# Kernel tuning notes

Hardware: AMD Instinct MI355X
Metric: run time of the kernel (lower is better)

## Reference

```python
import jax, jax.numpy as jnp
import numpy as np

B, S_LONG, S_SHORT, C_IN, H, D_STATE = 16384, 100, 10, 4, 64, 16
BN_EPS = 1e-5


def setup_inputs() -> dict:
    key = jax.random.key(0)
    ks = jax.random.split(key, 32)
    n = lambda i, shape, s=0.1: (jax.random.normal(ks[i], shape, dtype=jnp.float32) * s)
    inp = {
        "x": jax.random.normal(ks[0], (B, S_LONG, C_IN), dtype=jnp.float32),
        # ConvolutionalEyes (Conv1d weights are [out, in, k])
        "conv1_w": n(1, (H, C_IN, 3)), "conv1_b": n(2, (H,)),
        "conv2_w": n(3, (H, H, 5)),    "conv2_b": n(4, (H,)),
        "conv3_w": n(5, (H, H, 7)),    "conv3_b": n(6, (H,)),
        # BatchNorm1d (eval mode: running_mean=0, running_var=1)
        "bn1_g": jnp.ones((H,)), "bn1_b": jnp.zeros((H,)),
        "bn2_g": jnp.ones((H,)), "bn2_b": jnp.zeros((H,)),
        "bn3_g": jnp.ones((H,)), "bn3_b": jnp.zeros((H,)),
        # input_proj
        "proj_w": n(7, (C_IN, H)), "proj_b": n(8, (H,)),
        # MambaBlock (proj_in exists in torch code but is unused in forward)
        "A": n(9, (D_STATE, D_STATE)),
        "Bm": n(10, (H, D_STATE)),
        "Cm": n(11, (D_STATE, H)),
        "out_w": n(12, (H, H)), "out_b": n(13, (H,)),
        # ContextualGate
        "g1_w": n(14, (2 * H, H)), "g1_b": n(15, (H,)),
        "g2_w": n(16, (H, H)),     "g2_b": n(17, (H,)),
        # trading head
        "h1_w": n(18, (H, 32)), "h1_b": n(19, (32,)),
        "h2_w": n(20, (32, 3)), "h2_b": n(21, (3,)),
    }
    return inp


def _conv_bn_relu(x, w, b, g, beta, pad):
    # x: [B, C, L], w: [O, I, K]
    y = jax.lax.conv_general_dilated(x, w, (1,), [(pad, pad)],
                                     dimension_numbers=("NCW", "OIW", "NCW"))
    y = y + b[None, :, None]
    # eval-mode BN with running_mean=0, running_var=1
    y = g[None, :, None] * y * jax.lax.rsqrt(jnp.float32(1.0 + BN_EPS)) + beta[None, :, None]
    return jax.nn.relu(y)


def reference(x, conv1_w, conv1_b, conv2_w, conv2_b, conv3_w, conv3_b,
              bn1_g, bn1_b, bn2_g, bn2_b, bn3_g, bn3_b,
              proj_w, proj_b, A, Bm, Cm, out_w, out_b,
              g1_w, g1_b, g2_w, g2_b, h1_w, h1_b, h2_w, h2_b):
    # --- split windows ---
    x_short = x[:, -S_SHORT:, :]          # [B, 10, 4]
    x_long = x                            # [B, 100, 4]

    # --- ConvolutionalEyes (dropout = identity in eval) ---
    xc = jnp.swapaxes(x_short, 1, 2)      # [B, 4, 10]
    xc = _conv_bn_relu(xc, conv1_w, conv1_b, bn1_g, bn1_b, 1)
    xc = _conv_bn_relu(xc, conv2_w, conv2_b, bn2_g, bn2_b, 2)
    xc = _conv_bn_relu(xc, conv3_w, conv3_b, bn3_g, bn3_b, 3)
    short_features = jnp.mean(xc, axis=2)  # [B, 64]

    # --- input projection ---
    xp = x_long @ proj_w + proj_b          # [B, 100, 64]

    # --- MambaBlock: sequential scan over time ---
    def step(h, x_t):                      # h: [B, 16], x_t: [B, 64]
        h = jnp.tanh(x_t @ Bm + h @ A.T)
        return h, h @ Cm                   # y_t: [B, 64]

    h0 = jnp.zeros((x.shape[0], D_STATE), dtype=x.dtype)
    _, ys = jax.lax.scan(step, h0, jnp.swapaxes(xp, 0, 1))  # ys: [100, B, 64]
    long_context = ys[-1] @ out_w + out_b  # proj_out applied, last timestep

    # --- ContextualGate ---
    combined = jnp.concatenate([short_features, long_context], axis=1)  # [B, 128]
    gate = jax.nn.sigmoid(jnp.tanh(combined @ g1_w + g1_b) @ g2_w + g2_b)
    filtered = short_features * gate

    # --- trading head (dropout = identity in eval) ---
    logits = jax.nn.relu(filtered @ h1_w + h1_b) @ h2_w + h2_b  # [B, 3]
    return logits
```

## Files before the change

### kernel.cpp

```cpp
#include <hip/hip_runtime.h>
#include <cstddef>

#define NB 16384
#define NRNN (NB/64)

typedef __attribute__((ext_vector_type(8))) _Float16 half8;
typedef __attribute__((ext_vector_type(4))) _Float16 half4;
typedef __attribute__((ext_vector_type(4))) float f32x4;
typedef __attribute__((ext_vector_type(2))) float f32x2;
typedef __attribute__((ext_vector_type(16))) float f32x16;

#define OFF_W1T 0
#define OFF_SC1 768
#define OFF_SH1 832
#define OFF_SC2 896
#define OFF_SH2 960
#define OFF_SC3 1024
#define OFF_SH3 1088
#define OFF_PB  1152
#define OFF_PBB 1216
#define OFF_W2H 2304
#define OFF_W2L 12544
#define OFF_W3H 22784
#define OFF_W3L 37120
#define OFF_SF  51456
#define OFF_H   (51456 + NB*64)
#define OFF_TF  1362176

#define G1H 0
#define G1L 8192
#define G2H 16384
#define G2L 20480
#define H1H 24576
#define H1L 26624
#define H2H 28672
#define H2L 29184
#define COH 29696
#define COL 30720
#define TFH 31744

static __device__ __forceinline__ f32x16 mfma32(half8 a, half8 b, f32x16 c) {
  return __builtin_amdgcn_mfma_f32_32x32x16_f16(a, b, c, 0, 0, 0);
}
static __device__ __forceinline__ f32x4 mfma16(half4 a, half4 b, f32x4 c) {
  return __builtin_amdgcn_mfma_f32_16x16x16f16(a, b, c, 0, 0, 0);
}
static __device__ __forceinline__ f32x4 mfma16k32(half8 a, half8 b, f32x4 c) {
  return __builtin_amdgcn_mfma_f32_16x16x32_f16(a, b, c, 0, 0, 0);
}

__global__ __launch_bounds__(256) void prep_kernel(
    const float* __restrict__ conv1_w, const float* __restrict__ conv1_b,
    const float* __restrict__ conv2_w, const float* __restrict__ conv2_b,
    const float* __restrict__ conv3_w, const float* __restrict__ conv3_b,
    const float* __restrict__ bn1_g, const float* __restrict__ bn1_b,
    const float* __restrict__ bn2_g, const float* __restrict__ bn2_b,
    const float* __restrict__ bn3_g, const float* __restrict__ bn3_b,
    const float* __restrict__ proj_w, const float* __restrict__ proj_b,
    const float* __restrict__ A, const float* __restrict__ Bm,
    const float* __restrict__ Cm, const float* __restrict__ out_w,
    const float* __restrict__ g1_w, const float* __restrict__ g2_w,
    const float* __restrict__ h1_w, const float* __restrict__ h2_w,
    float* __restrict__ ws)
{
  int tid = blockIdx.x * blockDim.x + threadIdx.x;
  int nt = gridDim.x * blockDim.x;
  const float s = rsqrtf(1.0f + 1e-5f);

  for (int i = tid; i < 64*12; i += nt) {
    int o = i & 63, rk = i >> 6;
    ws[OFF_W1T + i] = conv1_w[o*12 + rk];
  }
  for (int o = tid; o < 64; o += nt) {
    float s1 = bn1_g[o]*s, s2 = bn2_g[o]*s, s3 = bn3_g[o]*s;
    ws[OFF_SC1+o] = s1; ws[OFF_SH1+o] = s1*conv1_b[o] + bn1_b[o];
    ws[OFF_SC2+o] = s2; ws[OFF_SH2+o] = s2*conv2_b[o] + bn2_b[o];
    ws[OFF_SC3+o] = s3; ws[OFF_SH3+o] = s3*conv3_b[o] + bn3_b[o];
  }
  {
    _Float16* w2h = (_Float16*)(ws + OFF_W2H);
    _Float16* w2l = (_Float16*)(ws + OFF_W2L);
    for (int i = tid; i < 20*2*64; i += nt) {
      int lane = i & 63, ot = (i >> 6) & 1, sk = i >> 7;
      int tap = sk >> 2, ic0 = (sk & 3)*16 + (lane >> 5)*8;
      int o = ot*32 + (lane & 31);
      #pragma unroll
      for (int j = 0; j < 8; ++j) {
        float w = conv2_w[o*320 + (ic0 + j)*5 + tap];
        _Float16 hi = (_Float16)w;
        w2h[(size_t)i*8 + j] = hi;
        w2l[(size_t)i*8 + j] = (_Float16)(w - (float)hi);
      }
    }
  }
  {
    _Float16* w3h = (_Float16*)(ws + OFF_W3H);
    _Float16* w3l = (_Float16*)(ws + OFF_W3L);
    for (int i = tid; i < 28*2*64; i += nt) {
      int lane = i & 63, ot = (i >> 6) & 1, sk = i >> 7;
      int tap = sk >> 2, ic0 = (sk & 3)*16 + (lane >> 5)*8;
      int o = ot*32 + (lane & 31);
      #pragma unroll
      for (int j = 0; j < 8; ++j) {
        float w = conv3_w[o*448 + (ic0 + j)*7 + tap];
        _Float16 hi = (_Float16)w;
        w3h[(size_t)i*8 + j] = hi;
        w3l[(size_t)i*8 + j] = (_Float16)(w - (float)hi);
      }
    }
  }
  for (int i = tid; i < 64; i += nt) {
    int c = i >> 4, j = i & 15;
    float acc = 0.f;
    for (int m = 0; m < 64; ++m) acc += proj_w[c*64+m]*Bm[m*16+j];
    ws[OFF_PB + i] = acc;
  }
  for (int j = tid; j < 16; j += nt) {
    float acc = 0.f;
    for (int m = 0; m < 64; ++m) acc += proj_b[m]*Bm[m*16+j];
    ws[OFF_PBB + j] = acc;
  }

  _Float16* tf = (_Float16*)(ws + OFF_TF);
  for (int i = tid; i < 16*64; i += nt) {
    int l = i & 63, f = i >> 6, mt = f >> 2, ks = f & 3;
    int o = mt*16 + (l & 15), kb = ks*32 + (l >> 4)*8;
    #pragma unroll
    for (int j = 0; j < 8; ++j) {
      float w = g1_w[(size_t)(kb + j)*64 + o];
      _Float16 hi = (_Float16)w;
      tf[G1H + (size_t)i*8 + j] = hi;
      tf[G1L + (size_t)i*8 + j] = (_Float16)(w - (float)hi);
    }
  }
  for (int i = tid; i < 8*64; i += nt) {
    int l = i & 63, f = i >> 6, mt = f >> 1, ks = f & 1;
    int o = mt*16 + (l & 15), kb = ks*32 + (l >> 4)*8;
    #pragma unroll
    for (int j = 0; j < 8; ++j) {
      float w = g2_w[(size_t)(kb + j)*64 + o];
      _Float16 hi = (_Float16)w;
      tf[G2H + (size_t)i*8 + j] = hi;
      tf[G2L + (size_t)i*8 + j] = (_Float16)(w - (float)hi);
    }
  }
  for (int i = tid; i < 4*64; i += nt) {
    int l = i & 63, f = i >> 6, mt = f >> 1, ks = f & 1;
    int hx = mt*16 + (l & 15), kb = ks*32 + (l >> 4)*8;
    #pragma unroll
    for (int j = 0; j < 8; ++j) {
      float w = h1_w[(size_t)(kb + j)*32 + hx];
      _Float16 hi = (_Float16)w;
      tf[H1H + (size_t)i*8 + j] = hi;
      tf[H1L + (size_t)i*8 + j] = (_Float16)(w - (float)hi);
    }
  }
  for (int i = tid; i < 64; i += nt) {
    int l = i, m = l & 15, kb = (l >> 4)*8;
    #pragma unroll
    for (int j = 0; j < 8; ++j) {
      float w = (m < 3) ? h2_w[(size_t)(kb + j)*3 + m] : 0.f;
      _Float16 hi = (_Float16)w;
      tf[H2H + (size_t)i*8 + j] = hi;
      tf[H2L + (size_t)i*8 + j] = (_Float16)(w - (float)hi);
    }
  }
  for (int i = tid; i < 4*64; i += nt) {
    int l = i & 63, mt = i >> 6;
    int o = mt*16 + (l & 15), kb = (l >> 4)*4;
    #pragma unroll
    for (int j = 0; j < 4; ++j) {
      float acc = 0.f;
      for (int m = 0; m < 64; ++m) acc += Cm[(kb + j)*64 + m]*out_w[m*64 + o];
      _Float16 hi = (_Float16)acc;
      tf[COH + (size_t)i*4 + j] = hi;
      tf[COL + (size_t)i*4 + j] = (_Float16)(acc - (float)hi);
    }
  }
}

__global__ __launch_bounds__(256, 4) void conv123_kernel(
    const float* __restrict__ x, const float* __restrict__ wsr,
    const float* __restrict__ A, float* __restrict__ hout,
    float* __restrict__ sfp)
{
  __shared__ __align__(16) _Float16 ah[16][640], al[16][640];

  const int tid = threadIdx.x;
  const int lane = tid & 63;
  const int wid = tid >> 6;

  if (blockIdx.x < NRNN) {
    const int colb = lane & 15;
    const int q = lane >> 4;
    const size_t b = ((size_t)blockIdx.x*4 + wid)*16 + colb;

    const f32x4 av = *(const f32x4*)(A + (size_t)(lane & 15)*16 + q*4);
    half4 Ahi, Alo;
    #pragma unroll
    for (int j = 0; j < 4; ++j) {
      _Float16 hi = (_Float16)av[j];
      Ahi[j] = hi;
      Alo[j] = (_Float16)(av[j] - (float)hi);
    }
    f32x4 pb0 = *(const f32x4*)(wsr + OFF_PB + 0*16 + q*4);
    f32x4 pb1 = *(const f32x4*)(wsr + OFF_PB + 1*16 + q*4);
    f32x4 pb2 = *(const f32x4*)(wsr + OFF_PB + 2*16 + q*4);
    f32x4 pb3 = *(const f32x4*)(wsr + OFF_PB + 3*16 + q*4);
    f32x4 pbb = *(const f32x4*)(wsr + OFF_PBB + q*4);

    const float* xb = x + b*400;
    half4 hh = {}, hl = {};
    f32x4 hf;
    #pragma unroll 4
    for (int t = 0; t < 100; ++t) {
      const f32x4 xv = *(const f32x4*)(xb + t*4);
      f32x4 U;
      #pragma unroll
      for (int r = 0; r < 4; ++r)
        U[r] = pbb[r] + xv[0]*pb0[r] + xv[1]*pb1[r] + xv[2]*pb2[r] + xv[3]*pb3[r];
      f32x4 u = mfma16(Alo, hh, U);
      u = mfma16(Ahi, hl, u);
      u = mfma16(Ahi, hh, u);
      #pragma unroll
      for (int r = 0; r < 4; ++r) {
        float e = __expf(2.f*u[r]);
        float hn = 1.f - 2.f/(e + 1.f);
        hf[r] = hn;
        _Float16 hi = (_Float16)hn;
        hh[r] = hi;
        hl[r] = (_Float16)(hn - (float)hi);
      }
    }
    *(f32x4*)(hout + b*16 + q*4) = hf;
    return;
  }

  const int n = lane & 15;
  const int nc = (n < 10) ? n : 9;
  const int cbK = (lane >> 5);
  const int rq = 4 * (lane >> 5);
  const int lbA = 4*wid + ((lane >> 4) & 1);
  const int lbB = lbA + 2;
  const half8 z8 = {};
  const size_t B0g = (size_t)(blockIdx.x - NRNN) * 16;

  {
    const float sc1 = wsr[OFF_SC1 + lane], sh1 = wsr[OFF_SH1 + lane];
    const int lc = lane >> 3, lo7 = lane & 7;
    #pragma unroll
    for (int bb = 0; bb < 4; ++bb) {
      const int lb = 4*wid + bb;
      const size_t gb = B0g + lb;
      float xv[4][12];
      #pragma unroll
      for (int c = 0; c < 4; ++c) { xv[c][0] = 0.f; xv[c][11] = 0.f; }
      #pragma unroll
      for (int tt = 0; tt < 10; ++tt) {
        const f32x4 xt = *(const f32x4*)(x + gb*400 + (90 + tt)*4);
        #pragma unroll
        for (int c = 0; c < 4; ++c) xv[c][1 + tt] = xt[c];
      }
      float a1[10];
      #pragma unroll
      for (int t = 0; t < 10; ++t) a1[t] = 0.f;
      #pragma unroll
      for (int c = 0; c < 4; ++c)
        #pragma unroll
        for (int k = 0; k < 3; ++k) {
          const float wv = wsr[OFF_W1T + (c*3 + k)*64 + lane];
          #pragma unroll
          for (int t = 0; t < 10; ++t) a1[t] += wv * xv[c][t + k];
        }
      #pragma unroll
      for (int t = 0; t < 10; ++t) {
        float v = sc1*a1[t] + sh1;
        v = v > 0.f ? v : 0.f;
        _Float16 hi = (_Float16)v;
        const int sw = t*64 + (((lc ^ (t & 7)) << 3) | lo7);
        ah[lb][sw] = hi;
        al[lb][sw] = (_Float16)(v - (float)hi);
      }
    }
  }

  const _Float16* bhpA = &ah[lbA][0];
  const _Float16* blpA = &al[lbA][0];
  const _Float16* bhpB = &ah[lbB][0];
  const _Float16* blpB = &al[lbB][0];
  const _Float16* w2h = (const _Float16*)(wsr + OFF_W2H);
  const _Float16* w2l = (const _Float16*)(wsr + OFF_W2L);
  const _Float16* w3h = (const _Float16*)(wsr + OFF_W3H);
  const _Float16* w3l = (const _Float16*)(wsr + OFF_W3L);
  const int lw8 = lane*8;

  f32x16 a0A, a1A, a0B, a1B;
  {
    #pragma unroll
    for (int r = 0; r < 16; ++r) { a0A[r] = 0.f; a1A[r] = 0.f; a0B[r] = 0.f; a1B[r] = 0.f; }
    #pragma unroll
    for (int sk = 0; sk < 20; ++sk) {
      const int tap = sk >> 2;
      const int cb = (sk & 3)*2 + cbK;
      const int t = nc + tap - 2;
      const int tc = t < 0 ? 0 : (t > 9 ? 9 : t);
      const bool valid = (t >= 0) & (t <= 9);
      const int off = tc*64 + ((cb ^ (tc & 7)) << 3);
      half8 bhA = *(const half8*)(bhpA + off);
      half8 blA = *(const half8*)(blpA + off);
      half8 bhB = *(const half8*)(bhpB + off);
      half8 blB = *(const half8*)(blpB + off);
      bhA = valid ? bhA : z8;
      blA = valid ? blA : z8;
      bhB = valid ? bhB : z8;
      blB = valid ? blB : z8;
      const half8 wh0 = *(const half8*)(w2h + (size_t)(sk*2 + 0)*512 + lw8);
      const half8 wh1 = *(const half8*)(w2h + (size_t)(sk*2 + 1)*512 + lw8);
      const half8 wl0 = *(const half8*)(w2l + (size_t)(sk*2 + 0)*512 + lw8);
      const half8 wl1 = *(const half8*)(w2l + (size_t)(sk*2 + 1)*512 + lw8);
      a0A = mfma32(wh0, bhA, a0A);
      a0A = mfma32(wh0, blA, a0A);
      a0A = mfma32(wl0, bhA, a0A);
      a1A = mfma32(wh1, bhA, a1A);
      a1A = mfma32(wh1, blA, a1A);
      a1A = mfma32(wl1, bhA, a1A);
      a0B = mfma32(wh0, bhB, a0B);
      a0B = mfma32(wh0, blB, a0B);
      a0B = mfma32(wl0, bhB, a0B);
      a1B = mfma32(wh1, bhB, a1B);
      a1B = mfma32(wh1, blB, a1B);
      a1B = mfma32(wl1, bhB, a1B);
    }
    if (n < 10) {
      const int n7 = n & 7;
      auto epi = [&](const f32x16& ac, int ot, int lb) {
        #pragma unroll
        for (int q = 0; q < 4; ++q) {
          const int rowb = 8*q + rq + ot*32;
          const f32x4 sc = *(const f32x4*)(wsr + OFF_SC2 + rowb);
          const f32x4 sh = *(const f32x4*)(wsr + OFF_SH2 + rowb);
          half4 h4, l4;
          #pragma unroll
          for (int r = 0; r < 4; ++r) {
            float v = sc[r]*ac[4*q + r] + sh[r];
            v = v > 0.f ? v : 0.f;
            _Float16 hi = (_Float16)v;
            h4[r] = hi;
            l4[r] = (_Float16)(v - (float)hi);
          }
          const int sw = n*64 + (((((q + 4*ot) ^ n7)) << 3) | rq);
          *(half4*)(&ah[lb][sw]) = h4;
          *(half4*)(&al[lb][sw]) = l4;
        }
      };
      epi(a0A, 0, lbA);
      epi(a1A, 1, lbA);
      epi(a0B, 0, lbB);
      epi(a1B, 1, lbB);
    }
  }

  {
    f32x16 b0A, b1A, b0B, b1B;
    #pragma unroll
    for (int r = 0; r < 16; ++r) { b0A[r] = 0.f; b1A[r] = 0.f; b0B[r] = 0.f; b1B[r] = 0.f; }
    #pragma unroll
    for (int sk = 0; sk < 28; ++sk) {
      const int tap = sk >> 2;
      const int cb = (sk & 3)*2 + cbK;
      const int t = nc + tap - 3;
      const int tc = t < 0 ? 0 : (t > 9 ? 9 : t);
      const bool valid = (t >= 0) & (t <= 9);
      const int off = tc*64 + ((cb ^ (tc & 7)) << 3);
      half8 bhA = *(const half8*)(bhpA + off);
      half8 blA = *(const half8*)(blpA + off);
      half8 bhB = *(const half8*)(bhpB + off);
      half8 blB = *(const half8*)(blpB + off);
      bhA = valid ? bhA : z8;
      blA = valid ? blA : z8;
      bhB = valid ? bhB : z8;
      blB = valid ? blB : z8;
      const half8 wh0 = *(const half8*)(w3h + (size_t)(sk*2 + 0)*512 + lw8);
      const half8 wh1 = *(const half8*)(w3h + (size_t)(sk*2 + 1)*512 + lw8);
      const half8 wl0 = *(const half8*)(w3l + (size_t)(sk*2 + 0)*512 + lw8);
      const half8 wl1 = *(const half8*)(w3l + (size_t)(sk*2 + 1)*512 + lw8);
      b0A = mfma32(wh0, bhA, b0A);
      b0A = mfma32(wh0, blA, b0A);
      b0A = mfma32(wl0, bhA, b0A);
      b1A = mfma32(wh1, bhA, b1A);
      b1A = mfma32(wh1, blA, b1A);
      b1A = mfma32(wl1, bhA, b1A);
      b0B = mfma32(wh0, bhB, b0B);
      b0B = mfma32(wh0, blB, b0B);
      b0B = mfma32(wl0, bhB, b0B);
      b1B = mfma32(wh1, bhB, b1B);
      b1B = mfma32(wh1, blB, b1B);
      b1B = mfma32(wl1, bhB, b1B);
    }
    auto epi = [&](const f32x16& ac, int ot, int lb) {
      #pragma unroll
      for (int q = 0; q < 4; ++q) {
        const int rowb = 8*q + rq + ot*32;
        const f32x4 sc = *(const f32x4*)(wsr + OFF_SC3 + rowb);
        const f32x4 sh = *(const f32x4*)(wsr + OFF_SH3 + rowb);
        f32x4 v;
        #pragma unroll
        for (int r = 0; r < 4; ++r) {
          float t2 = sc[r]*ac[4*q + r] + sh[r];
          t2 = t2 > 0.f ? t2 : 0.f;
          v[r] = (n < 10) ? t2 : 0.f;
        }
        #pragma unroll
        for (int r = 0; r < 4; ++r) {
          v[r] += __shfl_xor(v[r], 1, 16);
          v[r] += __shfl_xor(v[r], 2, 16);
          v[r] += __shfl_xor(v[r], 4, 16);
          v[r] += __shfl_xor(v[r], 8, 16);
        }
        if (n == 0)
          *(f32x4*)(sfp + (B0g + lb)*64 + rowb) = v * 0.1f;
      }
    };
    epi(b0A, 0, lbA);
    epi(b1A, 1, lbA);
    epi(b0B, 0, lbB);
    epi(b1B, 1, lbB);
  }
}

#define CMBH 0
#define CMBL 2176
#define T1H  4352
#define T1L  5504
#define FLH  6656
#define FLL  7808
#define RH   8960
#define RL   9600
__global__ __launch_bounds__(256) void tail_kernel(
    const float* __restrict__ wsr,
    const float* __restrict__ g1_b, const float* __restrict__ g2_b,
    const float* __restrict__ h1_b, const float* __restrict__ h2_b,
    const float* __restrict__ out_b, float* __restrict__ out)
{
  __shared__ __align__(16) _Float16 sWF[TFH];
  __shared__ __align__(16) _Float16 sAct[4*10240];

  const int tid = threadIdx.x;
  const int lane = tid & 63;
  const int wid = tid >> 6;
  const int n = lane & 15;
  const int q = lane >> 4;
  const int B0 = blockIdx.x*64 + wid*16;

  {
    const f32x4* src = (const f32x4*)(wsr + OFF_TF);
    f32x4* dst = (f32x4*)sWF;
    for (int i = tid; i < TFH/8; i += 256) dst[i] = src[i];
  }
  __syncthreads();

  _Float16* wa = sAct + wid*10240;
  const float* sf = wsr + OFF_SF;
  const float* hws = wsr + OFF_H;

  const f32x4 hv = *(const f32x4*)(hws + (size_t)(B0 + n)*16 + q*4);
  half4 hh, hl;
  #pragma unroll
  for (int j = 0; j < 4; ++j) {
    _Float16 hi = (_Float16)hv[j];
    hh[j] = hi;
    hl[j] = (_Float16)(hv[j] - (float)hi);
  }
  f32x4 lc[4];
  #pragma unroll
  for (int mt = 0; mt < 4; ++mt) {
    lc[mt] = *(const f32x4*)(out_b + mt*16 + q*4);
    const half4 ah = *(const half4*)(sWF + COH + (size_t)(mt*64 + lane)*4);
    const half4 al = *(const half4*)(sWF + COL + (size_t)(mt*64 + lane)*4);
    lc[mt] = mfma16(al, hh, lc[mt]);
    lc[mt] = mfma16(ah, hl, lc[mt]);
    lc[mt] = mfma16(ah, hh, lc[mt]);
  }
  f32x4 sfv[4];
  #pragma unroll
  for (int mt = 0; mt < 4; ++mt) {
    sfv[mt] = *(const f32x4*)(sf + (size_t)(B0 + n)*64 + mt*16 + q*4);
    half4 sh4, sl4, lh4, ll4;
    #pragma unroll
    for (int r = 0; r < 4; ++r) {
      _Float16 hi = (_Float16)sfv[mt][r];
      sh4[r] = hi; sl4[r] = (_Float16)(sfv[mt][r] - (float)hi);
      _Float16 hi2 = (_Float16)lc[mt][r];
      lh4[r] = hi2; ll4[r] = (_Float16)(lc[mt][r] - (float)hi2);
    }
    *(half4*)(wa + CMBH + n*136 + mt*16 + q*4) = sh4;
    *(half4*)(wa + CMBL + n*136 + mt*16 + q*4) = sl4;
    *(half4*)(wa + CMBH + n*136 + 64 + mt*16 + q*4) = lh4;
    *(half4*)(wa + CMBL + n*136 + 64 + mt*16 + q*4) = ll4;
  }
  f32x4 u1[4];
  #pragma unroll
  for (int mt = 0; mt < 4; ++mt) u1[mt] = *(const f32x4*)(g1_b + mt*16 + q*4);
  #pragma unroll
  for (int ks = 0; ks < 4; ++ks) {
    const half8 bh = *(const half8*)(wa + CMBH + n*136 + ks*32 + q*8);
    const half8 bl = *(const half8*)(wa + CMBL + n*136 + ks*32 + q*8);
    #pragma unroll
    for (int mt = 0; mt < 4; ++mt) {
      const half8 ah = *(const half8*)(sWF + G1H + (size_t)((mt*4 + ks)*64 + lane)*8);
      const half8 al = *(const half8*)(sWF + G1L + (size_t)((mt*4 + ks)*64 + lane)*8);
      u1[mt] = mfma16k32(al, bh, u1[mt]);
      u1[mt] = mfma16k32(ah, bl, u1[mt]);
      u1[mt] = mfma16k32(ah, bh, u1[mt]);
    }
  }
  #pragma unroll
  for (int mt = 0; mt < 4; ++mt) {
    half4 th4, tl4;
    #pragma unroll
    for (int r = 0; r < 4; ++r) {
      float e = __expf(2.f*u1[mt][r]);
      float t1 = 1.f - 2.f/(e + 1.f);
      _Float16 hi = (_Float16)t1;
      th4[r] = hi; tl4[r] = (_Float16)(t1 - (float)hi);
    }
    *(half4*)(wa + T1H + n*72 + mt*16 + q*4) = th4;
    *(half4*)(wa + T1L + n*72 + mt*16 + q*4) = tl4;
  }
  f32x4 u2[4];
  #pragma unroll
  for (int mt = 0; mt < 4; ++mt) u2[mt] = *(const f32x4*)(g2_b + mt*16 + q*4);
  #pragma unroll
  for (int ks = 0; ks < 2; ++ks) {
    const half8 bh = *(const half8*)(wa + T1H + n*72 + ks*32 + q*8);
    const half8 bl = *(const half8*)(wa + T1L + n*72 + ks*32 + q*8);
    #pragma unroll
    for (int mt = 0; mt < 4; ++mt) {
      const half8 ah = *(const half8*)(sWF + G2H + (size_t)((mt*2 + ks)*64 + lane)*8);
      const half8 al = *(const half8*)(sWF + G2L + (size_t)((mt*2 + ks)*64 + lane)*8);
      u2[mt] = mfma16k32(al, bh, u2[mt]);
      u2[mt] = mfma16k32(ah, bl, u2[mt]);
      u2[mt] = mfma16k32(ah, bh, u2[mt]);
    }
  }
  #pragma unroll
  for (int mt = 0; mt < 4; ++mt) {
    half4 fh4, fl4;
    #pragma unroll
    for (int r = 0; r < 4; ++r) {
      float gate = 1.f/(1.f + __expf(-u2[mt][r]));
      float f = sfv[mt][r] * gate;
      _Float16 hi = (_Float16)f;
      fh4[r] = hi; fl4[r] = (_Float16)(f - (float)hi);
    }
    *(half4*)(wa + FLH + n*72 + mt*16 + q*4) = fh4;
    *(half4*)(wa + FLL + n*72 + mt*16 + q*4) = fl4;
  }
  f32x4 u3[2];
  #pragma unroll
  for (int mt = 0; mt < 2; ++mt) u3[mt] = *(const f32x4*)(h1_b + mt*16 + q*4);
  #pragma unroll
  for (int ks = 0; ks < 2; ++ks) {
    const half8 bh = *(const half8*)(wa + FLH + n*72 + ks*32 + q*8);
    const half8 bl = *(const half8*)(wa + FLL + n*72 + ks*32 + q*8);
    #pragma unroll
    for (int mt = 0; mt < 2; ++mt) {
      const half8 ah = *(const half8*)(sWF + H1H + (size_t)((mt*2 + ks)*64 + lane)*8);
      const half8 al = *(const half8*)(sWF + H1L + (size_t)((mt*2 + ks)*64 + lane)*8);
      u3[mt] = mfma16k32(al, bh, u3[mt]);
      u3[mt] = mfma16k32(ah, bl, u3[mt]);
      u3[mt] = mfma16k32(ah, bh, u3[mt]);
    }
  }
  #pragma unroll
  for (int mt = 0; mt < 2; ++mt) {
    half4 rh4, rl4;
    #pragma unroll
    for (int r = 0; r < 4; ++r) {
      float v = fmaxf(u3[mt][r], 0.f);
      _Float16 hi = (_Float16)v;
      rh4[r] = hi; rl4[r] = (_Float16)(v - (float)hi);
    }
    *(half4*)(wa + RH + n*40 + mt*16 + q*4) = rh4;
    *(half4*)(wa + RL + n*40 + mt*16 + q*4) = rl4;
  }
  {
    f32x4 u4;
    if (q == 0) { u4[0] = h2_b[0]; u4[1] = h2_b[1]; u4[2] = h2_b[2]; u4[3] = 0.f; }
    else { u4[0] = 0.f; u4[1] = 0.f; u4[2] = 0.f; u4[3] = 0.f; }
    const half8 bh = *(const half8*)(wa + RH + n*40 + q*8);
    const half8 bl = *(const half8*)(wa + RL + n*40 + q*8);
    const half8 ah = *(const half8*)(sWF + H2H + (size_t)lane*8);
    const half8 al = *(const half8*)(sWF + H2L + (size_t)lane*8);
    u4 = mfma16k32(al, bh, u4);
    u4 = mfma16k32(ah, bl, u4);
    u4 = mfma16k32(ah, bh, u4);
    if (q == 0) {
      out[(size_t)(B0 + n)*3 + 0] = u4[0];
      out[(size_t)(B0 + n)*3 + 1] = u4[1];
      out[(size_t)(B0 + n)*3 + 2] = u4[2];
    }
  }
}

extern "C" void kernel_launch(void* const* d_in, const int* in_sizes, int n_in,
                              void* d_out, int out_size, void* d_ws, size_t ws_size,
                              hipStream_t stream) {
  const float* x       = (const float*)d_in[0];
  const float* conv1_w = (const float*)d_in[1];
  const float* conv1_b = (const float*)d_in[2];
  const float* conv2_w = (const float*)d_in[3];
  const float* conv2_b = (const float*)d_in[4];
  const float* conv3_w = (const float*)d_in[5];
  const float* conv3_b = (const float*)d_in[6];
  const float* bn1_g   = (const float*)d_in[7];
  const float* bn1_b   = (const float*)d_in[8];
  const float* bn2_g   = (const float*)d_in[9];
  const float* bn2_b   = (const float*)d_in[10];
  const float* bn3_g   = (const float*)d_in[11];
  const float* bn3_b   = (const float*)d_in[12];
  const float* proj_w  = (const float*)d_in[13];
  const float* proj_b  = (const float*)d_in[14];
  const float* A       = (const float*)d_in[15];
  const float* Bm      = (const float*)d_in[16];
  const float* Cm      = (const float*)d_in[17];
  const float* out_w   = (const float*)d_in[18];
  const float* out_b   = (const float*)d_in[19];
  const float* g1_w    = (const float*)d_in[20];
  const float* g1_b    = (const float*)d_in[21];
  const float* g2_w    = (const float*)d_in[22];
  const float* g2_b    = (const float*)d_in[23];
  const float* h1_w    = (const float*)d_in[24];
  const float* h1_b    = (const float*)d_in[25];
  const float* h2_w    = (const float*)d_in[26];
  const float* h2_b    = (const float*)d_in[27];
  float* ws = (float*)d_ws;
  float* out = (float*)d_out;

  prep_kernel<<<64, 256, 0, stream>>>(conv1_w, conv1_b, conv2_w, conv2_b,
      conv3_w, conv3_b, bn1_g, bn1_b, bn2_g, bn2_b, bn3_g, bn3_b,
      proj_w, proj_b, A, Bm, Cm, out_w, g1_w, g2_w, h1_w, h2_w, ws);

  conv123_kernel<<<NRNN + NB/16, 256, 0, stream>>>(x, ws, A, ws + OFF_H,
      ws + OFF_SF);

  tail_kernel<<<NB/64, 256, 0, stream>>>(ws, g1_b, g2_b, h1_b, h2_b, out_b, out);
}
```

Before: 243.0 us.

## Fold RNN scan into conv blocks and switch LDS swizzle to additive rotation

Removes the separate RNN blocks and instead runs the 100-step recurrence for each conv block's 16 batch rows on wave 0 after the conv stages, so the grid shrinks to NB/16 blocks. The LDS swizzle changes from XOR to an additive rotation that depends on the batch pair, meant to reduce bank conflicts, and the conv1 input loads become scalar per-channel. The risk is a serialized tail in which only one wave of each block runs the long scan while the other three waves sit idle.

```diff
diff --git a/kernel.cpp b/kernel.cpp
--- a/kernel.cpp
+++ b/kernel.cpp
@@ -2,7 +2,6 @@
 #include <cstddef>
 
 #define NB 16384
-#define NRNN (NB/64)
 
 typedef __attribute__((ext_vector_type(8))) _Float16 half8;
 typedef __attribute__((ext_vector_type(4))) _Float16 half4;
@@ -190,112 +189,65 @@
   const int lane = tid & 63;
   const int wid = tid >> 6;
 
-  if (blockIdx.x < NRNN) {
-    const int colb = lane & 15;
-    const int q = lane >> 4;
-    const size_t b = ((size_t)blockIdx.x*4 + wid)*16 + colb;
-
-    const f32x4 av = *(const f32x4*)(A + (size_t)(lane & 15)*16 + q*4);
-    half4 Ahi, Alo;
-    #pragma unroll
-    for (int j = 0; j < 4; ++j) {
-      _Float16 hi = (_Float16)av[j];
-      Ahi[j] = hi;
-      Alo[j] = (_Float16)(av[j] - (float)hi);
-    }
-    f32x4 pb0 = *(const f32x4*)(wsr + OFF_PB + 0*16 + q*4);
-    f32x4 pb1 = *(const f32x4*)(wsr + OFF_PB + 1*16 + q*4);
-    f32x4 pb2 = *(const f32x4*)(wsr + OFF_PB + 2*16 + q*4);
-    f32x4 pb3 = *(const f32x4*)(wsr + OFF_PB + 3*16 + q*4);
-    f32x4 pbb = *(const f32x4*)(wsr + OFF_PBB + q*4);
-
-    const float* xb = x + b*400;
-    half4 hh = {}, hl = {};
-    f32x4 hf;
-    #pragma unroll 4
-    for (int t = 0; t < 100; ++t) {
-      const f32x4 xv = *(const f32x4*)(xb + t*4);
-      f32x4 U;
-      #pragma unroll
-      for (int r = 0; r < 4; ++r)
-        U[r] = pbb[r] + xv[0]*pb0[r] + xv[1]*pb1[r] + xv[2]*pb2[r] + xv[3]*pb3[r];
-      f32x4 u = mfma16(Alo, hh, U);
-      u = mfma16(Ahi, hl, u);
-      u = mfma16(Ahi, hh, u);
-      #pragma unroll
-      for (int r = 0; r < 4; ++r) {
-        float e = __expf(2.f*u[r]);
-        float hn = 1.f - 2.f/(e + 1.f);
-        hf[r] = hn;
-        _Float16 hi = (_Float16)hn;
-        hh[r] = hi;
-        hl[r] = (_Float16)(hn - (float)hi);
-      }
-    }
-    *(f32x4*)(hout + b*16 + q*4) = hf;
-    return;
-  }
-
   const int n = lane & 15;
   const int nc = (n < 10) ? n : 9;
   const int cbK = (lane >> 5);
   const int rq = 4 * (lane >> 5);
-  const int lbA = 4*wid + ((lane >> 4) & 1);
+  const int pairsel = (lane >> 4) & 1;
+  const int lbA = 4*wid + pairsel;
   const int lbB = lbA + 2;
+  const int rA = lbA*640, rB = lbB*640;
+  const int twA = 2*pairsel;
+  const int twB = twA + 4;
   const half8 z8 = {};
-  const size_t B0g = (size_t)(blockIdx.x - NRNN) * 16;
+  const size_t B0g = (size_t)blockIdx.x * 16;
 
   {
     const float sc1 = wsr[OFF_SC1 + lane], sh1 = wsr[OFF_SH1 + lane];
-    const int lc = lane >> 3, lo7 = lane & 7;
+    const int lc8 = lane >> 3, lo7 = lane & 7;
     #pragma unroll
     for (int bb = 0; bb < 4; ++bb) {
       const int lb = 4*wid + bb;
       const size_t gb = B0g + lb;
-      float xv[4][12];
-      #pragma unroll
-      for (int c = 0; c < 4; ++c) { xv[c][0] = 0.f; xv[c][11] = 0.f; }
-      #pragma unroll
-      for (int tt = 0; tt < 10; ++tt) {
-        const f32x4 xt = *(const f32x4*)(x + gb*400 + (90 + tt)*4);
+      float a1[10];
+      #pragma unroll
+      for (int t = 0; t < 10; ++t) a1[t] = 0.f;
+      #pragma unroll
+      for (int c = 0; c < 4; ++c) {
+        float xc[12];
+        xc[0] = 0.f; xc[11] = 0.f;
         #pragma unroll
-        for (int c = 0; c < 4; ++c) xv[c][1 + tt] = xt[c];
-      }
-      float a1[10];
-      #pragma unroll
-      for (int t = 0; t < 10; ++t) a1[t] = 0.f;
-      #pragma unroll
-      for (int c = 0; c < 4; ++c)
+        for (int tt = 0; tt < 10; ++tt)
+          xc[1 + tt] = x[gb*400 + (90 + tt)*4 + c];
         #pragma unroll
         for (int k = 0; k < 3; ++k) {
           const float wv = wsr[OFF_W1T + (c*3 + k)*64 + lane];
           #pragma unroll
-          for (int t = 0; t < 10; ++t) a1[t] += wv * xv[c][t + k];
+          for (int t = 0; t < 10; ++t) a1[t] += wv * xc[t + k];
         }
+      }
       #pragma unroll
       for (int t = 0; t < 10; ++t) {
         float v = sc1*a1[t] + sh1;
         v = v > 0.f ? v : 0.f;
         _Float16 hi = (_Float16)v;
-        const int sw = t*64 + (((lc ^ (t & 7)) << 3) | lo7);
+        const int sw = t*64 + (((lc8 + t + 2*bb) & 7) << 3) + lo7;
         ah[lb][sw] = hi;
         al[lb][sw] = (_Float16)(v - (float)hi);
       }
     }
   }
 
-  const _Float16* bhpA = &ah[lbA][0];
-  const _Float16* blpA = &al[lbA][0];
-  const _Float16* bhpB = &ah[lbB][0];
-  const _Float16* blpB = &al[lbB][0];
+  const _Float16* abase = &ah[0][0];
+  const _Float16* lbase = &al[0][0];
   const _Float16* w2h = (const _Float16*)(wsr + OFF_W2H);
   const _Float16* w2l = (const _Float16*)(wsr + OFF_W2L);
   const _Float16* w3h = (const _Float16*)(wsr + OFF_W3H);
   const _Float16* w3l = (const _Float16*)(wsr + OFF_W3L);
   const int lw8 = lane*8;
 
-  f32x16 a0A, a1A, a0B, a1B;
   {
+    f32x16 a0A, a1A, a0B, a1B;
     #pragma unroll
     for (int r = 0; r < 16; ++r) { a0A[r] = 0.f; a1A[r] = 0.f; a0B[r] = 0.f; a1B[r] = 0.f; }
     #pragma unroll
@@ -305,11 +257,13 @@
       const int t = nc + tap - 2;
       const int tc = t < 0 ? 0 : (t > 9 ? 9 : t);
       const bool valid = (t >= 0) & (t <= 9);
-      const int off = tc*64 + ((cb ^ (tc & 7)) << 3);
-      half8 bhA = *(const half8*)(bhpA + off);
-      half8 blA = *(const half8*)(blpA + off);
-      half8 bhB = *(const half8*)(bhpB + off);
-      half8 blB = *(const half8*)(blpB + off);
+      const int s = cb + tc;
+      const int offA = rA + tc*64 + (((s + twA) & 7) << 3);
+      const int offB = rB + tc*64 + (((s + twB) & 7) << 3);
+      half8 bhA = *(const half8*)(abase + offA);
+      half8 blA = *(const half8*)(lbase + offA);
+      half8 bhB = *(const half8*)(abase + offB);
+      half8 blB = *(const half8*)(lbase + offB);
       bhA = valid ? bhA : z8;
       blA = valid ? blA : z8;
       bhB = valid ? bhB : z8;
@@ -332,8 +286,8 @@
       a1B = mfma32(wl1, bhB, a1B);
     }
     if (n < 10) {
-      const int n7 = n & 7;
       auto epi = [&](const f32x16& ac, int ot, int lb) {
+        const int tw = 2*(lb & 3);
         #pragma unroll
         for (int q = 0; q < 4; ++q) {
           const int rowb = 8*q + rq + ot*32;
@@ -348,7 +302,7 @@
             h4[r] = hi;
             l4[r] = (_Float16)(v - (float)hi);
           }
-          const int sw = n*64 + (((((q + 4*ot) ^ n7)) << 3) | rq);
+          const int sw = n*64 + ((((q + 4*ot) + n + tw) & 7) << 3) + rq;
           *(half4*)(&ah[lb][sw]) = h4;
           *(half4*)(&al[lb][sw]) = l4;
         }
@@ -371,11 +325,13 @@
       const int t = nc + tap - 3;
       const int tc = t < 0 ? 0 : (t > 9 ? 9 : t);
       const bool valid = (t >= 0) & (t <= 9);
-      const int off = tc*64 + ((cb ^ (tc & 7)) << 3);
-      half8 bhA = *(const half8*)(bhpA + off);
-      half8 blA = *(const half8*)(blpA + off);
-      half8 bhB = *(const half8*)(bhpB + off);
-      half8 blB = *(const half8*)(blpB + off);
+      const int s = cb + tc;
+      const int offA = rA + tc*64 + (((s + twA) & 7) << 3);
+      const int offB = rB + tc*64 + (((s + twB) & 7) << 3);
+      half8 bhA = *(const half8*)(abase + offA);
+      half8 blA = *(const half8*)(lbase + offA);
+      half8 bhB = *(const half8*)(abase + offB);
+      half8 blB = *(const half8*)(lbase + offB);
       bhA = valid ? bhA : z8;
       blA = valid ? blA : z8;
       bhB = valid ? bhB : z8;
@@ -425,6 +381,51 @@
     epi(b1A, 1, lbA);
     epi(b0B, 0, lbB);
     epi(b1B, 1, lbB);
+  }
+
+  if (wid == 0) {
+    const int colb = lane & 15;
+    const int qr = lane >> 4;
+    const size_t b = B0g + colb;
+
+    const f32x4 av = *(const f32x4*)(A + (size_t)colb*16 + qr*4);
+    half4 Ahi, Alo;
+    #pragma unroll
+    for (int j = 0; j < 4; ++j) {
+      _Float16 hi = (_Float16)av[j];
+      Ahi[j] = hi;
+      Alo[j] = (_Float16)(av[j] - (float)hi);
+    }
+    f32x4 pb0 = *(const f32x4*)(wsr + OFF_PB + 0*16 + qr*4);
+    f32x4 pb1 = *(const f32x4*)(wsr + OFF_PB + 1*16 + qr*4);
+    f32x4 pb2 = *(const f32x4*)(wsr + OFF_PB + 2*16 + qr*4);
+    f32x4 pb3 = *(const f32x4*)(wsr + OFF_PB + 3*16 + qr*4);
+    f32x4 pbb = *(const f32x4*)(wsr + OFF_PBB + qr*4);
+
+    const float* xb = x + b*400;
+    half4 hh = {}, hl = {};
+    f32x4 hf;
+    #pragma unroll 2
+    for (int t = 0; t < 100; ++t) {
+      const f32x4 xv = *(const f32x4*)(xb + t*4);
+      f32x4 U;
+      #pragma unroll
+      for (int r = 0; r < 4; ++r)
+        U[r] = pbb[r] + xv[0]*pb0[r] + xv[1]*pb1[r] + xv[2]*pb2[r] + xv[3]*pb3[r];
+      f32x4 u = mfma16(Alo, hh, U);
+      u = mfma16(Ahi, hl, u);
+      u = mfma16(Ahi, hh, u);
+      #pragma unroll
+      for (int r = 0; r < 4; ++r) {
+        float e = __expf(2.f*u[r]);
+        float hn = 1.f - 2.f/(e + 1.f);
+        hf[r] = hn;
+        _Float16 hi = (_Float16)hn;
+        hh[r] = hi;
+        hl[r] = (_Float16)(hn - (float)hi);
+      }
+    }
+    *(f32x4*)(hout + b*16 + qr*4) = hf;
   }
 }
 
@@ -641,7 +642,7 @@
       conv3_w, conv3_b, bn1_g, bn1_b, bn2_g, bn2_b, bn3_g, bn3_b,
       proj_w, proj_b, A, Bm, Cm, out_w, g1_w, g2_w, h1_w, h2_w, ws);
 
-  conv123_kernel<<<NRNN + NB/16, 256, 0, stream>>>(x, ws, A, ws + OFF_H,
+  conv123_kernel<<<NB/16, 256, 0, stream>>>(x, ws, A, ws + OFF_H,
       ws + OFF_SF);
 
   tail_kernel<<<NB/64, 256, 0, stream>>>(ws, g1_b, g2_b, h1_b, h2_b, out_b, out);
```

Measured after the change: 257.0 us. +5.7%, slower.

## Replace XOR-swizzled conv LDS layout with padded rows; read tail weights from global

Applied to the files above, without the earlier changes.

The conv activation tile in shared memory moves from an XOR-swizzled 64-wide row layout to a padded 72-element row stride, which simplifies address math while still avoiding bank conflicts. The tail kernel stops staging its fp16 weight tables into shared memory and reads them directly from global memory (L1/L2), removing a copy and a block barrier. Launch bounds and the RNN loop unroll factor are also retuned. The padded layout uses more LDS, which lowers the occupancy target for conv blocks, and the tail's weight loads now depend on cache hits.

```diff
diff --git a/kernel.cpp b/kernel.cpp
--- a/kernel.cpp
+++ b/kernel.cpp
@@ -2,6 +2,7 @@
 #include <cstddef>
 
 #define NB 16384
+#define TS 720
 #define NRNN (NB/64)
 
 typedef __attribute__((ext_vector_type(8))) _Float16 half8;
@@ -179,12 +180,12 @@
   }
 }
 
-__global__ __launch_bounds__(256, 4) void conv123_kernel(
+__global__ __launch_bounds__(256, 3) void conv123_kernel(
     const float* __restrict__ x, const float* __restrict__ wsr,
     const float* __restrict__ A, float* __restrict__ hout,
     float* __restrict__ sfp)
 {
-  __shared__ __align__(16) _Float16 ah[16][640], al[16][640];
+  __shared__ __align__(16) _Float16 ah[16][TS], al[16][TS];
 
   const int tid = threadIdx.x;
   const int lane = tid & 63;
@@ -212,7 +213,7 @@
     const float* xb = x + b*400;
     half4 hh = {}, hl = {};
     f32x4 hf;
-    #pragma unroll 4
+    #pragma unroll 2
     for (int t = 0; t < 100; ++t) {
       const f32x4 xv = *(const f32x4*)(xb + t*4);
       f32x4 U;
@@ -238,7 +239,7 @@
 
   const int n = lane & 15;
   const int nc = (n < 10) ? n : 9;
-  const int cbK = (lane >> 5);
+  const int kh8 = (lane >> 5) * 8;
   const int rq = 4 * (lane >> 5);
   const int lbA = 4*wid + ((lane >> 4) & 1);
   const int lbB = lbA + 2;
@@ -247,7 +248,6 @@
 
   {
     const float sc1 = wsr[OFF_SC1 + lane], sh1 = wsr[OFF_SH1 + lane];
-    const int lc = lane >> 3, lo7 = lane & 7;
     #pragma unroll
     for (int bb = 0; bb < 4; ++bb) {
       const int lb = 4*wid + bb;
@@ -277,9 +277,8 @@
         float v = sc1*a1[t] + sh1;
         v = v > 0.f ? v : 0.f;
         _Float16 hi = (_Float16)v;
-        const int sw = t*64 + (((lc ^ (t & 7)) << 3) | lo7);
-        ah[lb][sw] = hi;
-        al[lb][sw] = (_Float16)(v - (float)hi);
+        ah[lb][t*72 + lane] = hi;
+        al[lb][t*72 + lane] = (_Float16)(v - (float)hi);
       }
     }
   }
@@ -294,18 +293,17 @@
   const _Float16* w3l = (const _Float16*)(wsr + OFF_W3L);
   const int lw8 = lane*8;
 
-  f32x16 a0A, a1A, a0B, a1B;
   {
+    f32x16 a0A, a1A, a0B, a1B;
     #pragma unroll
     for (int r = 0; r < 16; ++r) { a0A[r] = 0.f; a1A[r] = 0.f; a0B[r] = 0.f; a1B[r] = 0.f; }
     #pragma unroll
     for (int sk = 0; sk < 20; ++sk) {
-      const int tap = sk >> 2;
-      const int cb = (sk & 3)*2 + cbK;
+      const int tap = sk >> 2, icb = (sk & 3)*16;
       const int t = nc + tap - 2;
       const int tc = t < 0 ? 0 : (t > 9 ? 9 : t);
       const bool valid = (t >= 0) & (t <= 9);
-      const int off = tc*64 + ((cb ^ (tc & 7)) << 3);
+      const int off = tc*72 + icb + kh8;
       half8 bhA = *(const half8*)(bhpA + off);
       half8 blA = *(const half8*)(blpA + off);
       half8 bhB = *(const half8*)(bhpB + off);
@@ -332,7 +330,6 @@
       a1B = mfma32(wl1, bhB, a1B);
     }
     if (n < 10) {
-      const int n7 = n & 7;
       auto epi = [&](const f32x16& ac, int ot, int lb) {
         #pragma unroll
         for (int q = 0; q < 4; ++q) {
@@ -348,9 +345,8 @@
             h4[r] = hi;
             l4[r] = (_Float16)(v - (float)hi);
           }
-          const int sw = n*64 + (((((q + 4*ot) ^ n7)) << 3) | rq);
-          *(half4*)(&ah[lb][sw]) = h4;
-          *(half4*)(&al[lb][sw]) = l4;
+          *(half4*)(&ah[lb][n*72 + rowb]) = h4;
+          *(half4*)(&al[lb][n*72 + rowb]) = l4;
         }
       };
       epi(a0A, 0, lbA);
@@ -366,12 +362,11 @@
     for (int r = 0; r < 16; ++r) { b0A[r] = 0.f; b1A[r] = 0.f; b0B[r] = 0.f; b1B[r] = 0.f; }
     #pragma unroll
     for (int sk = 0; sk < 28; ++sk) {
-      const int tap = sk >> 2;
-      const int cb = (sk & 3)*2 + cbK;
+      const int tap = sk >> 2, icb = (sk & 3)*16;
       const int t = nc + tap - 3;
       const int tc = t < 0 ? 0 : (t > 9 ? 9 : t);
       const bool valid = (t >= 0) & (t <= 9);
-      const int off = tc*64 + ((cb ^ (tc & 7)) << 3);
+      const int off = tc*72 + icb + kh8;
       half8 bhA = *(const half8*)(bhpA + off);
       half8 blA = *(const half8*)(blpA + off);
       half8 bhB = *(const half8*)(bhpB + off);
@@ -436,13 +431,12 @@
 #define FLL  7808
 #define RH   8960
 #define RL   9600
-__global__ __launch_bounds__(256) void tail_kernel(
+__global__ __launch_bounds__(256, 2) void tail_kernel(
     const float* __restrict__ wsr,
     const float* __restrict__ g1_b, const float* __restrict__ g2_b,
     const float* __restrict__ h1_b, const float* __restrict__ h2_b,
     const float* __restrict__ out_b, float* __restrict__ out)
 {
-  __shared__ __align__(16) _Float16 sWF[TFH];
   __shared__ __align__(16) _Float16 sAct[4*10240];
 
   const int tid = threadIdx.x;
@@ -452,13 +446,7 @@
   const int q = lane >> 4;
   const int B0 = blockIdx.x*64 + wid*16;
 
-  {
-    const f32x4* src = (const f32x4*)(wsr + OFF_TF);
-    f32x4* dst = (f32x4*)sWF;
-    for (int i = tid; i < TFH/8; i += 256) dst[i] = src[i];
-  }
-  __syncthreads();
-
+  const _Float16* tfg = (const _Float16*)(wsr + OFF_TF);
   _Float16* wa = sAct + wid*10240;
   const float* sf = wsr + OFF_SF;
   const float* hws = wsr + OFF_H;
@@ -475,8 +463,8 @@
   #pragma unroll
   for (int mt = 0; mt < 4; ++mt) {
     lc[mt] = *(const f32x4*)(out_b + mt*16 + q*4);
-    const half4 ah = *(const half4*)(sWF + COH + (size_t)(mt*64 + lane)*4);
-    const half4 al = *(const half4*)(sWF + COL + (size_t)(mt*64 + lane)*4);
+    const half4 ah = *(const half4*)(tfg + COH + (size_t)(mt*64 + lane)*4);
+    const half4 al = *(const half4*)(tfg + COL + (size_t)(mt*64 + lane)*4);
     lc[mt] = mfma16(al, hh, lc[mt]);
     lc[mt] = mfma16(ah, hl, lc[mt]);
     lc[mt] = mfma16(ah, hh, lc[mt]);
@@ -507,8 +495,8 @@
     const half8 bl = *(const half8*)(wa + CMBL + n*136 + ks*32 + q*8);
     #pragma unroll
     for (int mt = 0; mt < 4; ++mt) {
-      const half8 ah = *(const half8*)(sWF + G1H + (size_t)((mt*4 + ks)*64 + lane)*8);
-      const half8 al = *(const half8*)(sWF + G1L + (size_t)((mt*4 + ks)*64 + lane)*8);
+      const half8 ah = *(const half8*)(tfg + G1H + (size_t)((mt*4 + ks)*64 + lane)*8);
+      const half8 al = *(const half8*)(tfg + G1L + (size_t)((mt*4 + ks)*64 + lane)*8);
       u1[mt] = mfma16k32(al, bh, u1[mt]);
       u1[mt] = mfma16k32(ah, bl, u1[mt]);
       u1[mt] = mfma16k32(ah, bh, u1[mt]);
@@ -536,8 +524,8 @@
     const half8 bl = *(const half8*)(wa + T1L + n*72 + ks*32 + q*8);
     #pragma unroll
     for (int mt = 0; mt < 4; ++mt) {
-      const half8 ah = *(const half8*)(sWF + G2H + (size_t)((mt*2 + ks)*64 + lane)*8);
-      const half8 al = *(const half8*)(sWF + G2L + (size_t)((mt*2 + ks)*64 + lane)*8);
+      const half8 ah = *(const half8*)(tfg + G2H + (size_t)((mt*2 + ks)*64 + lane)*8);
+      const half8 al = *(const half8*)(tfg + G2L + (size_t)((mt*2 + ks)*64 + lane)*8);
       u2[mt] = mfma16k32(al, bh, u2[mt]);
       u2[mt] = mfma16k32(ah, bl, u2[mt]);
       u2[mt] = mfma16k32(ah, bh, u2[mt]);
@@ -565,8 +553,8 @@
     const half8 bl = *(const half8*)(wa + FLL + n*72 + ks*32 + q*8);
     #pragma unroll
     for (int mt = 0; mt < 2; ++mt) {
-      const half8 ah = *(const half8*)(sWF + H1H + (size_t)((mt*2 + ks)*64 + lane)*8);
-      const half8 al = *(const half8*)(sWF + H1L + (size_t)((mt*2 + ks)*64 + lane)*8);
+      const half8 ah = *(const half8*)(tfg + H1H + (size_t)((mt*2 + ks)*64 + lane)*8);
+      const half8 al = *(const half8*)(tfg + H1L + (size_t)((mt*2 + ks)*64 + lane)*8);
       u3[mt] = mfma16k32(al, bh, u3[mt]);
       u3[mt] = mfma16k32(ah, bl, u3[mt]);
       u3[mt] = mfma16k32(ah, bh, u3[mt]);
@@ -590,8 +578,8 @@
     else { u4[0] = 0.f; u4[1] = 0.f; u4[2] = 0.f; u4[3] = 0.f; }
     const half8 bh = *(const half8*)(wa + RH + n*40 + q*8);
     const half8 bl = *(const half8*)(wa + RL + n*40 + q*8);
-    const half8 ah = *(const half8*)(sWF + H2H + (size_t)lane*8);
-    const half8 al = *(const half8*)(sWF + H2L + (size_t)lane*8);
+    const half8 ah = *(const half8*)(tfg + H2H + (size_t)lane*8);
+    const half8 al = *(const half8*)(tfg + H2L + (size_t)lane*8);
     u4 = mfma16k32(al, bh, u4);
     u4 = mfma16k32(ah, bl, u4);
     u4 = mfma16k32(ah, bh, u4);
```

Result: faster. 232.3 us (-4.4%).
